# Optimization experiments

Measured on AMD Instinct MI355X. Metric: run time of the kernel, lower is better.

Reference implementation:

```python
import jax, jax.numpy as jnp
import numpy as np

N_OBSERVED = 64
N_LATENT = 64
N_NODES = N_OBSERVED + N_LATENT
M = 2                # max parents per node (BA attachment param)
N_SAMPLES = 262144
CAL_N = 256
CAL_FRAC = 0.1
SIGMA_W = 1.0


def _build_dag():
    """BA-style DAG in topological order: node i picks min(M, i) earlier parents."""
    rng = np.random.default_rng(0)
    par_idx = np.zeros((N_NODES, M), np.int32)
    par_mask = np.zeros((N_NODES, M), np.float32)
    is_root = np.zeros(N_NODES, bool)
    for i in range(N_NODES):
        k = min(M, i)
        if k == 0:
            is_root[i] = True
            continue
        ps = rng.choice(i, size=k, replace=False)
        par_idx[i, :k] = ps
        par_mask[i, :k] = 1.0
    has_child = np.zeros(N_NODES, bool)
    for i in range(N_NODES):
        for j in range(M):
            if par_mask[i, j] > 0:
                has_child[par_idx[i, j]] = True
    leaves = np.where(~has_child)[0]
    pool = leaves if len(leaves) >= N_OBSERVED else np.arange(N_NODES)
    chosen = rng.choice(pool, size=N_OBSERVED, replace=False).astype(np.int32)
    return par_idx, par_mask, is_root, chosen


def setup_inputs() -> dict:
    par_idx, par_mask, is_root, chosen = _build_dag()
    wrng = np.random.default_rng(1)
    n_par = par_mask.sum(axis=1)
    std = SIGMA_W / np.sqrt(np.maximum(n_par, 1.0))  # nn.init.normal_(std=sigma_w/sqrt(n_parents))
    W = (wrng.standard_normal((N_NODES, M)) * std[:, None] * par_mask).astype(np.float32)
    b = np.zeros(N_NODES, np.float32)                # bias zero-initialised
    key = jax.random.key(0)
    k1, k2, k3 = jax.random.split(key, 3)
    return {
        "n_samples": N_SAMPLES,
        "W": jnp.asarray(W),
        "b": jnp.asarray(b),
        "root_pilot": jax.random.normal(k1, (N_NODES, CAL_N), jnp.float32),
        "root_main": jax.random.normal(k2, (N_NODES, N_SAMPLES), jnp.float32),
        "z_noise": jax.random.normal(k3, (N_NODES, N_SAMPLES), jnp.float32),
        "par_mask": jnp.asarray(par_mask),
        "par_idx": jnp.asarray(par_idx),
        "is_root": jnp.asarray(is_root),
        "chosen": jnp.asarray(chosen),
    }


def _run_dag(W, b, par_mask, par_idx, is_root, roots, noise):
    """Topological scan: x_i = relu(w_i . x_parents + b_i) + noise_i, roots ~ given."""
    n = roots.shape[1]

    def step(vals, inp):
        i, pidx, pmask, w, bb, root_v, nz, rt = inp
        pv = vals[pidx]                                   # [M, n] gather parents
        h = jax.nn.relu(jnp.einsum("p,pn->n", w * pmask, pv) + bb) + nz
        v = jnp.where(rt, root_v, h)
        v = jnp.where(jnp.isfinite(v), v, jnp.zeros_like(v))
        vals = jax.lax.dynamic_update_slice(vals, v[None, :], (i, 0))
        return vals, None

    vals0 = jnp.zeros((N_NODES, n), roots.dtype)
    xs = (jnp.arange(N_NODES), par_idx, par_mask, W, b, roots, noise, is_root)
    vals, _ = jax.lax.scan(step, vals0, xs)
    return vals


def reference(n_samples, W, b, root_pilot, root_main, z_noise, par_mask, par_idx, is_root, chosen):
    # noise calibration: noiseless pilot pass, sigma_e = frac * IQR per node
    pilot = _run_dag(W, b, par_mask, par_idx, is_root, root_pilot, jnp.zeros_like(root_pilot))
    q75 = jnp.quantile(pilot, 0.75, axis=1)
    q25 = jnp.quantile(pilot, 0.25, axis=1)
    sigma_e = CAL_FRAC * jnp.maximum(q75 - q25, 1e-6)     # [N_NODES]
    # main pass with calibrated per-node noise
    vals = _run_dag(W, b, par_mask, par_idx, is_root, root_main, z_noise * sigma_e[:, None])
    return vals[chosen].T                                  # [n_samples, n_observed]
```

## Files before the change

### kernel.cpp

```cpp
#include <hip/hip_runtime.h>
#include <hip/hip_fp16.h>
#include <math.h>

#define NN   128
#define BS   64
#define SCAP 1056
#define RT_F 0x10000

#define IDX(n,t) ((n)*BS + ((t) ^ (((n)&15)<<1)))


__global__ __launch_bounds__(128) void prep_kernel(
    const float* __restrict__ W, const float* __restrict__ b,
    const float* __restrict__ pm, const int* __restrict__ pidx,
    float4* __restrict__ wtab, int* __restrict__ pcode,
    int* __restrict__ slotmap, int* __restrict__ ngp)
{
    __shared__ int grp[NN], slot[NN], wcnt[2];
    __shared__ int nassigned, gdone, gfin;
    const int i = threadIdx.x, w = i >> 6, lane = i & 63;
    const float m0 = pm[2*i], m1 = pm[2*i+1];
    const int   p0 = pidx[2*i], p1 = pidx[2*i+1];
    const int   rt = (m0 == 0.0f && m1 == 0.0f) ? 1 : 0;
    grp[i] = -1; slot[i] = 0;
    if (i == 0) { nassigned = 0; gdone = 0; gfin = 0; }
    __syncthreads();
    for (int g = 0; g < NN; ++g) {
        int ready = (grp[i] < 0) && (rt || (grp[p0] >= 0 && grp[p1] >= 0));
        unsigned long long mask = __ballot(ready);
        if (lane == 0) wcnt[w] = __popcll(mask);
        __syncthreads();
        int base = w ? wcnt[0] : 0;
        int r = base + __popcll(mask & ((1ull << lane) - 1ull));
        if (ready && r < 8) { grp[i] = g; slot[i] = g*8 + r; }
        if (i == 0) {
            nassigned += min(wcnt[0] + wcnt[1], 8);
            if (nassigned >= NN) { gdone = 1; gfin = g; }
        }
        __syncthreads();
        if (gdone) break;
    }
    const int S0 = 8 * (gfin + 1);
    const int S  = (S0 + 31) & ~31;
    for (int k = i; k < SCAP; k += NN) {
        pcode[k] = RT_F;
        wtab[k]  = make_float4(0.f, 0.f, 0.f, 0.f);
    }
    __threadfence_block();
    __syncthreads();
    pcode[slot[i]] = p0 | (p1 << 8) | (rt << 16) | (i << 24);
    wtab[slot[i]]  = make_float4(W[2*i]*m0, W[2*i+1]*m1, b[i], 0.f);
    slotmap[i] = slot[i];
    if (i == 0) ngp[0] = S;
}

__global__ __launch_bounds__(64) void pilot_kernel(
    const float4* __restrict__ wtab, const int* __restrict__ pcode,
    const int* __restrict__ ngp, const float* __restrict__ root_pilot,
    float* __restrict__ pilot_out, int CAL)
{
    __shared__ _Float16 vals[NN * BS];
    const int tid = threadIdx.x;
    const int jj  = blockIdx.x * BS + tid;
    const int S   = ngp[0];
    for (int s0 = 0; s0 < S; s0 += 8) {
        int pc[8]; float4 wv[8];
        #pragma unroll
        for (int u = 0; u < 8; ++u) pc[u] = pcode[s0 + u];
        #pragma unroll
        for (int u = 0; u < 8; ++u) wv[u] = wtab[s0 + u];
        #pragma unroll
        for (int u = 0; u < 8; ++u) {
            int node = (pc[u] >> 24) & 0xff;
            float v;
            if (pc[u] & RT_F) {
                v = root_pilot[node * CAL + jj];
            } else {
                int q0 = pc[u] & 0xff, q1 = (pc[u] >> 8) & 0xff;
                float a = (float)vals[IDX(q0, tid)];
                float c = (float)vals[IDX(q1, tid)];
                v = fmaxf(fmaf(wv[u].x, a, fmaf(wv[u].y, c, wv[u].z)), 0.0f);
            }
            if (!isfinite(v)) v = 0.0f;
            vals[IDX(node, tid)] = (_Float16)v;
            pilot_out[node * CAL + jj] = v;
        }
    }
}

__global__ __launch_bounds__(256) void quant_kernel(
    const float* __restrict__ pilot, const int* __restrict__ slotmap,
    float4* __restrict__ wtab, int CAL)
{
    __shared__ float s[256];
    const int tid = threadIdx.x;
    const int node = blockIdx.x;
    s[tid] = pilot[(size_t)node * CAL + tid];
    __syncthreads();
    for (int k = 2; k <= 256; k <<= 1) {
        for (int jj = k >> 1; jj > 0; jj >>= 1) {
            int ixj = tid ^ jj;
            if (ixj > tid) {
                float a = s[tid], bv = s[ixj];
                bool up = ((tid & k) == 0);
                if ((a > bv) == up) { s[tid] = bv; s[ixj] = a; }
            }
            __syncthreads();
        }
    }
    if (tid == 0) {
        float q25 = s[63]  + 0.75f * (s[64]  - s[63]);
        float q75 = s[191] + 0.25f * (s[192] - s[191]);
        ((float*)&wtab[slotmap[node]])[3] = 0.1f * fmaxf(q75 - q25, 1e-6f);
    }
}

__device__ __forceinline__ void mk_chunk(
    int c, int P, float (&zb)[2][16],
    const int* __restrict__ pcode, const float4* __restrict__ wtab,
    const float* __restrict__ root_main, const float* __restrict__ z,
    unsigned NS, size_t j, _Float16* vals, int tid)
{
    const int base = c * 16;
    #pragma unroll
    for (int u = 0; u < 16; ++u) {
        int pcN = pcode[base + 16 + u];
        const float* src = (pcN & RT_F) ? root_main : z;
        unsigned node = (unsigned)(pcN >> 24) & 0xffu;
        zb[P ^ 1][u] = src[(size_t)(node * NS) + j];
    }
    #pragma unroll
    for (int u = 0; u < 16; ++u) {
        int pc = pcode[base + u];
        float4 wv = wtab[base + u];
        float zv = zb[P][u];
        float v;
        if (pc & RT_F) {
            v = zv;
        } else {
            int q0 = pc & 0xff, q1 = (pc >> 8) & 0xff;
            float a  = (float)vals[IDX(q0, tid)];
            float c2 = (float)vals[IDX(q1, tid)];
            v = fmaxf(fmaf(wv.x, a, fmaf(wv.y, c2, wv.z)), 0.0f) + wv.w * zv;
        }
        if (!isfinite(v)) v = 0.0f;
        int node = (pc >> 24) & 0xff;
        vals[IDX(node, tid)] = (_Float16)v;
    }
}

__global__ __launch_bounds__(64) void main_kernel(
    const float4* __restrict__ wtab, const int* __restrict__ pcode,
    const int* __restrict__ ngp,
    const float* __restrict__ root_main, const float* __restrict__ z,
    const int* __restrict__ chosen, float* __restrict__ out, int NSi)
{
    __shared__ _Float16 vals[NN * BS];
    const int tid = threadIdx.x;
    const size_t j = (size_t)blockIdx.x * BS + tid;
    const unsigned NS = (unsigned)NSi;
    const int S = ngp[0];
    const int nch = S >> 4;

    float zb[2][16];
    #pragma unroll
    for (int u = 0; u < 16; ++u) {
        int pc = pcode[u];
        const float* src = (pc & RT_F) ? root_main : z;
        unsigned node = (unsigned)(pc >> 24) & 0xffu;
        zb[0][u] = src[(size_t)(node * NS) + j];
    }

    for (int c = 0; c < nch; c += 2) {
        mk_chunk(c,     0, zb, pcode, wtab, root_main, z, NS, j, vals, tid);
        mk_chunk(c + 1, 1, zb, pcode, wtab, root_main, z, NS, j, vals, tid);
    }

    __syncthreads();

    float4* out4 = (float4*)(out + (size_t)blockIdx.x * BS * 64);
    #pragma unroll
    for (int it = 0; it < 16; ++it) {
        int cc = it * BS + tid;
        int s  = cc >> 4;
        int k0 = (cc & 15) << 2;
        int n0 = chosen[k0], n1 = chosen[k0+1], n2 = chosen[k0+2], n3 = chosen[k0+3];
        float4 o;
        o.x = (float)vals[IDX(n0, s)];
        o.y = (float)vals[IDX(n1, s)];
        o.z = (float)vals[IDX(n2, s)];
        o.w = (float)vals[IDX(n3, s)];
        out4[cc] = o;
    }
}

extern "C" void kernel_launch(void* const* d_in, const int* in_sizes, int n_in,
                              void* d_out, int out_size, void* d_ws, size_t ws_size,
                              hipStream_t stream) {
    const float* W          = (const float*)d_in[1];
    const float* b          = (const float*)d_in[2];
    const float* root_pilot = (const float*)d_in[3];
    const float* root_main  = (const float*)d_in[4];
    const float* z          = (const float*)d_in[5];
    const float* pm         = (const float*)d_in[6];
    const int*   pidx       = (const int*)d_in[7];
    const int*   chosen     = (const int*)d_in[9];
    float* out = (float*)d_out;

    const int NS  = in_sizes[4] / NN;
    const int CAL = in_sizes[3] / NN;

    char* ws = (char*)d_ws;
    float4* wtab    = (float4*)ws;
    int*    pcode   = (int*)(ws + 20480);
    int*    slotmap = (int*)(ws + 24704);
    int*    ngp     = (int*)(ws + 25216);
    float*  pilot   = (float*)(ws + 28672);

    prep_kernel <<<1, 128, 0, stream>>>(W, b, pm, pidx, wtab, pcode, slotmap, ngp);
    pilot_kernel<<<CAL / BS, BS, 0, stream>>>(wtab, pcode, ngp, root_pilot, pilot, CAL);
    quant_kernel<<<NN, 256, 0, stream>>>(pilot, slotmap, wtab, CAL);
    main_kernel <<<NS / BS, BS, 0, stream>>>(wtab, pcode, ngp, root_main, z, chosen, out, NS);
}
```

Before: 350.6 us.

## Fuse prep and pilot kernels; batch LDS parent loads per 8-node group

Merges the prep and pilot kernels into one 256-thread single-block kernel, so the pilot pass runs inside the block that builds the level schedule. This removes a launch and the global round trip of the tables. In both the pilot and main kernels the per-node loop is split into phases: all 16 parent LDS reads for a group of 8 nodes are issued first, then the math, then all 8 writes, so LDS latency can overlap. The batching is only safe because nodes in one group of 8 do not depend on each other. The pilot pass now runs on one CU instead of four blocks, which may lengthen that serial stage.

```diff
diff --git a/kernel.cpp b/kernel.cpp
--- a/kernel.cpp
+++ b/kernel.cpp
@@ -10,31 +10,42 @@
 #define IDX(n,t) ((n)*BS + ((t) ^ (((n)&15)<<1)))
 
 
-__global__ __launch_bounds__(128) void prep_kernel(
+__global__ __launch_bounds__(256) void prep_pilot_kernel(
     const float* __restrict__ W, const float* __restrict__ b,
     const float* __restrict__ pm, const int* __restrict__ pidx,
+    const float* __restrict__ root_pilot,
     float4* __restrict__ wtab, int* __restrict__ pcode,
-    int* __restrict__ slotmap, int* __restrict__ ngp)
-{
-    __shared__ int grp[NN], slot[NN], wcnt[2];
+    int* __restrict__ slotmap, int* __restrict__ ngp,
+    float* __restrict__ pilot_out, int CAL)
+{
+    __shared__ _Float16 vals[NN * 256];
+    __shared__ int grp[NN], slot[NN], wcnt[4];
     __shared__ int nassigned, gdone, gfin;
     const int i = threadIdx.x, w = i >> 6, lane = i & 63;
-    const float m0 = pm[2*i], m1 = pm[2*i+1];
-    const int   p0 = pidx[2*i], p1 = pidx[2*i+1];
-    const int   rt = (m0 == 0.0f && m1 == 0.0f) ? 1 : 0;
-    grp[i] = -1; slot[i] = 0;
+
+    int p0 = 0, p1 = 0, rt = 1;
+    float m0 = 0.f, m1 = 0.f;
+    if (i < NN) {
+        m0 = pm[2*i]; m1 = pm[2*i+1];
+        p0 = pidx[2*i]; p1 = pidx[2*i+1];
+        rt = (m0 == 0.0f && m1 == 0.0f) ? 1 : 0;
+        grp[i] = -1; slot[i] = 0;
+    }
     if (i == 0) { nassigned = 0; gdone = 0; gfin = 0; }
     __syncthreads();
     for (int g = 0; g < NN; ++g) {
-        int ready = (grp[i] < 0) && (rt || (grp[p0] >= 0 && grp[p1] >= 0));
+        int ready = (i < NN) && (grp[i] < 0) && (rt || (grp[p0] >= 0 && grp[p1] >= 0));
         unsigned long long mask = __ballot(ready);
         if (lane == 0) wcnt[w] = __popcll(mask);
         __syncthreads();
-        int base = w ? wcnt[0] : 0;
+        int base = 0;
+        #pragma unroll
+        for (int ww = 0; ww < 4; ++ww) if (ww < w) base += wcnt[ww];
         int r = base + __popcll(mask & ((1ull << lane) - 1ull));
         if (ready && r < 8) { grp[i] = g; slot[i] = g*8 + r; }
         if (i == 0) {
-            nassigned += min(wcnt[0] + wcnt[1], 8);
+            int tot = wcnt[0] + wcnt[1] + wcnt[2] + wcnt[3];
+            nassigned += min(tot, 8);
             if (nassigned >= NN) { gdone = 1; gfin = g; }
         }
         __syncthreads();
@@ -42,48 +53,52 @@
     }
     const int S0 = 8 * (gfin + 1);
     const int S  = (S0 + 31) & ~31;
-    for (int k = i; k < SCAP; k += NN) {
+    for (int k = i; k < SCAP; k += 256) {
         pcode[k] = RT_F;
         wtab[k]  = make_float4(0.f, 0.f, 0.f, 0.f);
     }
     __threadfence_block();
     __syncthreads();
-    pcode[slot[i]] = p0 | (p1 << 8) | (rt << 16) | (i << 24);
-    wtab[slot[i]]  = make_float4(W[2*i]*m0, W[2*i+1]*m1, b[i], 0.f);
-    slotmap[i] = slot[i];
+    if (i < NN) {
+        pcode[slot[i]] = p0 | (p1 << 8) | (rt << 16) | (i << 24);
+        wtab[slot[i]]  = make_float4(W[2*i]*m0, W[2*i+1]*m1, b[i], 0.f);
+        slotmap[i] = slot[i];
+    }
     if (i == 0) ngp[0] = S;
-}
-
-__global__ __launch_bounds__(64) void pilot_kernel(
-    const float4* __restrict__ wtab, const int* __restrict__ pcode,
-    const int* __restrict__ ngp, const float* __restrict__ root_pilot,
-    float* __restrict__ pilot_out, int CAL)
-{
-    __shared__ _Float16 vals[NN * BS];
-    const int tid = threadIdx.x;
-    const int jj  = blockIdx.x * BS + tid;
-    const int S   = ngp[0];
+    __threadfence_block();
+    __syncthreads();
+
+    const int jj = i;
     for (int s0 = 0; s0 < S; s0 += 8) {
         int pc[8]; float4 wv[8];
         #pragma unroll
         for (int u = 0; u < 8; ++u) pc[u] = pcode[s0 + u];
         #pragma unroll
         for (int u = 0; u < 8; ++u) wv[u] = wtab[s0 + u];
-        #pragma unroll
-        for (int u = 0; u < 8; ++u) {
-            int node = (pc[u] >> 24) & 0xff;
+        float pa[8], pb[8];
+        #pragma unroll
+        for (int u = 0; u < 8; ++u) {
+            int q0 = pc[u] & 0xff, q1 = (pc[u] >> 8) & 0xff;
+            pa[u] = (float)vals[q0 * 256 + jj];
+            pb[u] = (float)vals[q1 * 256 + jj];
+        }
+        _Float16 res[8]; int nodes[8]; float vf[8];
+        #pragma unroll
+        for (int u = 0; u < 8; ++u) {
+            nodes[u] = (pc[u] >> 24) & 0xff;
             float v;
             if (pc[u] & RT_F) {
-                v = root_pilot[node * CAL + jj];
+                v = root_pilot[nodes[u] * CAL + jj];
             } else {
-                int q0 = pc[u] & 0xff, q1 = (pc[u] >> 8) & 0xff;
-                float a = (float)vals[IDX(q0, tid)];
-                float c = (float)vals[IDX(q1, tid)];
-                v = fmaxf(fmaf(wv[u].x, a, fmaf(wv[u].y, c, wv[u].z)), 0.0f);
+                v = fmaxf(fmaf(wv[u].x, pa[u], fmaf(wv[u].y, pb[u], wv[u].z)), 0.0f);
             }
             if (!isfinite(v)) v = 0.0f;
-            vals[IDX(node, tid)] = (_Float16)v;
-            pilot_out[node * CAL + jj] = v;
+            vf[u] = v; res[u] = (_Float16)v;
+        }
+        #pragma unroll
+        for (int u = 0; u < 8; ++u) {
+            vals[nodes[u] * 256 + jj] = res[u];
+            pilot_out[nodes[u] * CAL + jj] = vf[u];
         }
     }
 }
@@ -130,22 +145,34 @@
         zb[P ^ 1][u] = src[(size_t)(node * NS) + j];
     }
     #pragma unroll
-    for (int u = 0; u < 16; ++u) {
-        int pc = pcode[base + u];
-        float4 wv = wtab[base + u];
-        float zv = zb[P][u];
-        float v;
-        if (pc & RT_F) {
-            v = zv;
-        } else {
-            int q0 = pc & 0xff, q1 = (pc >> 8) & 0xff;
-            float a  = (float)vals[IDX(q0, tid)];
-            float c2 = (float)vals[IDX(q1, tid)];
-            v = fmaxf(fmaf(wv.x, a, fmaf(wv.y, c2, wv.z)), 0.0f) + wv.w * zv;
-        }
-        if (!isfinite(v)) v = 0.0f;
-        int node = (pc >> 24) & 0xff;
-        vals[IDX(node, tid)] = (_Float16)v;
+    for (int h = 0; h < 2; ++h) {
+        int pc[8];
+        #pragma unroll
+        for (int u = 0; u < 8; ++u) pc[u] = pcode[base + h*8 + u];
+        float pa[8], pb[8];
+        #pragma unroll
+        for (int u = 0; u < 8; ++u) {
+            int q0 = pc[u] & 0xff, q1 = (pc[u] >> 8) & 0xff;
+            pa[u] = (float)vals[IDX(q0, tid)];
+            pb[u] = (float)vals[IDX(q1, tid)];
+        }
+        _Float16 res[8]; int nodes[8];
+        #pragma unroll
+        for (int u = 0; u < 8; ++u) {
+            float4 wv = wtab[base + h*8 + u];
+            float zv = zb[P][h*8 + u];
+            float v;
+            if (pc[u] & RT_F) {
+                v = zv;
+            } else {
+                v = fmaxf(fmaf(wv.x, pa[u], fmaf(wv.y, pb[u], wv.z)), 0.0f) + wv.w * zv;
+            }
+            if (!isfinite(v)) v = 0.0f;
+            nodes[u] = (pc[u] >> 24) & 0xff;
+            res[u] = (_Float16)v;
+        }
+        #pragma unroll
+        for (int u = 0; u < 8; ++u) vals[IDX(nodes[u], tid)] = res[u];
     }
 }
 
@@ -217,8 +244,8 @@
     int*    ngp     = (int*)(ws + 25216);
     float*  pilot   = (float*)(ws + 28672);
 
-    prep_kernel <<<1, 128, 0, stream>>>(W, b, pm, pidx, wtab, pcode, slotmap, ngp);
-    pilot_kernel<<<CAL / BS, BS, 0, stream>>>(wtab, pcode, ngp, root_pilot, pilot, CAL);
+    prep_pilot_kernel<<<1, 256, 0, stream>>>(W, b, pm, pidx, root_pilot,
+                                             wtab, pcode, slotmap, ngp, pilot, CAL);
     quant_kernel<<<NN, 256, 0, stream>>>(pilot, slotmap, wtab, CAL);
     main_kernel <<<NS / BS, BS, 0, stream>>>(wtab, pcode, ngp, root_main, z, chosen, out, NS);
 }
```

Measured after the change: 337.9 us. -3.6%, faster.
